# Kernel optimization log

Hardware: AMD Instinct MI355X
Metric: run time of the kernel (lower is better)

The kernel has to match this reference:

```python
import jax, jax.numpy as jnp
import numpy as np

BN_EPS = 1e-3  # Keras BatchNormalization default epsilon

def _conv2d_same(x, w, b):
    # x: NHWC, w: HWIO (kh,kw,2,1)
    y = jax.lax.conv_general_dilated(x, w, window_strides=(1, 1), padding='SAME',
                                     dimension_numbers=('NHWC', 'HWIO', 'NHWC'))
    return y + b

def _zpool(t):
    # concat([max, avg], axis=-1) over channel axis -> last dim = 2
    return jnp.concatenate([jnp.max(t, axis=-1, keepdims=True),
                            jnp.mean(t, axis=-1, keepdims=True)], axis=-1)

def _att_map(t2, w, b, g, beta, mean, var):
    y = _conv2d_same(t2, w, b)
    y = (y - mean) * jax.lax.rsqrt(var + BN_EPS) * g + beta  # inference BN
    return jax.nn.sigmoid(y)

def setup_inputs() -> dict:
    key = jax.random.key(0)
    ks = jax.random.split(key, 8)
    B, H, W, C, K, RR = 32, 56, 56, 256, 7, 8
    d = {}
    d['x'] = jax.random.normal(ks[0], (B, H, W, C), dtype=jnp.float32)
    for i, kk in zip((1, 2, 3), ks[1:4]):
        d[f'conv{i}_w'] = jax.random.normal(kk, (K, K, 2, 1), dtype=jnp.float32) * 0.1
        d[f'conv{i}_b'] = jnp.zeros((1,), dtype=jnp.float32)
        d[f'bn{i}_g'] = jnp.ones((1,), dtype=jnp.float32)
        d[f'bn{i}_b'] = jnp.zeros((1,), dtype=jnp.float32)
        d[f'bn{i}_m'] = jnp.zeros((1,), dtype=jnp.float32)
        d[f'bn{i}_v'] = jnp.ones((1,), dtype=jnp.float32)
    Ch = C // RR
    d['se_w1'] = jax.random.normal(ks[4], (C, Ch), dtype=jnp.float32) * (2.0 / C) ** 0.5
    d['se_b1'] = jnp.zeros((Ch,), dtype=jnp.float32)
    d['se_w2'] = jax.random.normal(ks[5], (Ch, C), dtype=jnp.float32) * 0.05
    d['se_b2'] = jnp.zeros((C,), dtype=jnp.float32)
    return d

def reference(x, conv1_w, conv1_b, bn1_g, bn1_b, bn1_m, bn1_v,
              conv2_w, conv2_b, bn2_g, bn2_b, bn2_m, bn2_v,
              conv3_w, conv3_b, bn3_g, bn3_b, bn3_m, bn3_v,
              se_w1, se_b1, se_w2, se_b2):
    # Branch 1 (H-axis): permute (B,H,W,C)->(B,H,C,W), pool over W
    th1 = jnp.transpose(x, (0, 1, 3, 2))
    a1 = _att_map(_zpool(th1), conv1_w, conv1_b, bn1_g, bn1_b, bn1_m, bn1_v)
    br1 = jnp.transpose(th1 * a1, (0, 1, 3, 2))
    # Branch 2 (W-axis): permute (B,H,W,C)->(B,C,W,H), pool over H
    th2 = jnp.transpose(x, (0, 3, 2, 1))
    a2 = _att_map(_zpool(th2), conv2_w, conv2_b, bn2_g, bn2_b, bn2_m, bn2_v)
    br2 = jnp.transpose(th2 * a2, (0, 3, 2, 1))
    # Branch 3 (identity): pool over C
    a3 = _att_map(_zpool(x), conv3_w, conv3_b, bn3_g, bn3_b, bn3_m, bn3_v)
    br3 = x * a3
    # TriSE1: Add branches, then SE channel gating
    s = br1 + br2 + br3
    gap = jnp.mean(s, axis=(1, 2), keepdims=True)            # (B,1,1,C)
    h = jax.nn.relu(jnp.einsum('bijc,cd->bijd', gap, se_w1) + se_b1)
    cw = jax.nn.sigmoid(jnp.einsum('bijd,dc->bijc', h, se_w2) + se_b2)
    return s * cw
```

## Files before the change

### kernel.cpp

```cpp
#include <hip/hip_runtime.h>
#include <math.h>

namespace {
constexpr int B = 32, H = 56, W = 56, C = 256;
constexpr int HW  = H * W;
constexpr int WC  = W * C;
constexpr int HC  = H * C;
constexpr int HWC = H * W * C;
constexpr int CH  = 32;
constexpr float BN_EPS = 1e-3f;

__device__ __forceinline__ float sigmoidf_(float v) { return 1.0f / (1.0f + expf(-v)); }
}

__global__ __launch_bounds__(256)
void pool_all_kernel(const float* __restrict__ x,
                     float* __restrict__ pmax1, float* __restrict__ pavg1,
                     float* __restrict__ pmax2, float* __restrict__ pavg2,
                     float* __restrict__ pmax3, float* __restrict__ pavg3) {
    const int t = threadIdx.x;
    const int lane = t & 63, sub = t >> 6;
    const int c4 = lane * 4;
    __shared__ float smx[4][256];
    __shared__ float ssm[4][256];

    if (blockIdx.x < B * H) {
        const int b = blockIdx.x / H, h = blockIdx.x % H;
        const float* xp = x + (size_t)b * HWC + (size_t)h * WC + c4;
        float4 v[14];
        #pragma unroll
        for (int wq = 0; wq < 14; ++wq)
            v[wq] = *(const float4*)(xp + (wq * 4 + sub) * C);
        float4 mx = v[0], sm = v[0];
        #pragma unroll
        for (int wq = 1; wq < 14; ++wq) {
            mx.x = fmaxf(mx.x, v[wq].x); mx.y = fmaxf(mx.y, v[wq].y);
            mx.z = fmaxf(mx.z, v[wq].z); mx.w = fmaxf(mx.w, v[wq].w);
            sm.x += v[wq].x; sm.y += v[wq].y; sm.z += v[wq].z; sm.w += v[wq].w;
        }
        #pragma unroll
        for (int wq = 0; wq < 14; ++wq) {
            float m3 = fmaxf(fmaxf(v[wq].x, v[wq].y), fmaxf(v[wq].z, v[wq].w));
            float s3 = v[wq].x + v[wq].y + v[wq].z + v[wq].w;
            #pragma unroll
            for (int off = 32; off > 0; off >>= 1) {
                m3 = fmaxf(m3, __shfl_down(m3, off));
                s3 += __shfl_down(s3, off);
            }
            if (lane == 0) {
                const int w = wq * 4 + sub;
                pmax3[b * HW + h * W + w] = m3;
                pavg3[b * HW + h * W + w] = s3 * (1.0f / C);
            }
        }
        *(float4*)&smx[sub][c4] = mx;
        *(float4*)&ssm[sub][c4] = sm;
        __syncthreads();
        const float m = fmaxf(fmaxf(smx[0][t], smx[1][t]), fmaxf(smx[2][t], smx[3][t]));
        const float s = ssm[0][t] + ssm[1][t] + ssm[2][t] + ssm[3][t];
        pmax1[b * HC + h * C + t] = m;
        pavg1[b * HC + h * C + t] = s * (1.0f / W);
    } else {
        const int tt = blockIdx.x - B * H;
        const int b = tt / W, w = tt % W;
        const float* xp = x + (size_t)b * HWC + (size_t)w * C + c4;
        float4 v[14];
        #pragma unroll
        for (int i = 0; i < 14; ++i)
            v[i] = *(const float4*)(xp + (size_t)(i * 4 + sub) * WC);
        float4 mx = v[0], sm = v[0];
        #pragma unroll
        for (int i = 1; i < 14; ++i) {
            mx.x = fmaxf(mx.x, v[i].x); mx.y = fmaxf(mx.y, v[i].y);
            mx.z = fmaxf(mx.z, v[i].z); mx.w = fmaxf(mx.w, v[i].w);
            sm.x += v[i].x; sm.y += v[i].y; sm.z += v[i].z; sm.w += v[i].w;
        }
        *(float4*)&smx[sub][c4] = mx;
        *(float4*)&ssm[sub][c4] = sm;
        __syncthreads();
        const float m = fmaxf(fmaxf(smx[0][t], smx[1][t]), fmaxf(smx[2][t], smx[3][t]));
        const float s = ssm[0][t] + ssm[1][t] + ssm[2][t] + ssm[3][t];
        pmax2[(size_t)b * WC + w * C + t] = m;
        pavg2[(size_t)b * WC + w * C + t] = s * (1.0f / H);
    }
}

__global__ __launch_bounds__(256)
void conv_all_kernel(const float* __restrict__ x,
                     const float* __restrict__ pmax1, const float* __restrict__ pavg1,
                     const float* __restrict__ pmax2, const float* __restrict__ pavg2,
                     const float* __restrict__ pmax3, const float* __restrict__ pavg3,
                     const float* __restrict__ c1w, const float* __restrict__ c1b,
                     const float* __restrict__ g1,  const float* __restrict__ be1,
                     const float* __restrict__ m1,  const float* __restrict__ v1,
                     const float* __restrict__ c2w, const float* __restrict__ c2b,
                     const float* __restrict__ g2,  const float* __restrict__ be2,
                     const float* __restrict__ m2,  const float* __restrict__ v2,
                     const float* __restrict__ c3w, const float* __restrict__ c3b,
                     const float* __restrict__ g3,  const float* __restrict__ be3,
                     const float* __restrict__ m3,  const float* __restrict__ v3,
                     float* __restrict__ a1, float* __restrict__ a2t, float* __restrict__ a3,
                     float* __restrict__ gpart) {
    const int t = threadIdx.x;
    __shared__ float wg[98];
    __shared__ float2 sp[7][264];
    __shared__ float sa3[4][56];

    if (blockIdx.x < B * 14) {
        if (t < 98) wg[t] = c3w[t];
        float2 (*sp3)[66] = (float2(*)[66])sp;
        const int tt = blockIdx.x;
        const int b = tt / 14, h0 = (tt % 14) * 4;
        const float* bm = pmax3 + (size_t)b * HW;
        const float* ba = pavg3 + (size_t)b * HW;
        for (int idx = t; idx < 10 * 62; idx += 256) {
            const int r = idx / 62, col = idx % 62;
            const int hh = h0 + r - 3, ww = col - 3;
            const bool val = (hh >= 0 && hh < H && ww >= 0 && ww < W);
            const int hs = min(max(hh, 0), H - 1), wsx = min(max(ww, 0), W - 1);
            const float pm = bm[hs * W + wsx];
            const float pa = ba[hs * W + wsx];
            sp3[r][col] = val ? make_float2(pm, pa) : make_float2(0.f, 0.f);
        }
        __syncthreads();
        if (t < 224) {
            const int r = t / 56, w = t % 56;
            const float A  = rsqrtf(v3[0] + BN_EPS) * g3[0];
            const float Bc = (c3b[0] - m3[0]) * A + be3[0];
            float acc = 0.f;
            #pragma unroll
            for (int ky = 0; ky < 7; ++ky)
                #pragma unroll
                for (int kx = 0; kx < 7; ++kx) {
                    const float2 p = sp3[r + ky][w + kx];
                    acc += p.x * wg[ky * 14 + kx * 2] + p.y * wg[ky * 14 + kx * 2 + 1];
                }
            const float av = sigmoidf_(acc * A + Bc);
            a3[b * HW + (h0 + r) * W + w] = av;
            sa3[r][w] = av;
        }
        __syncthreads();
        const int lane = t & 63, sub = t >> 6;
        const int c4 = lane * 4;
        const float* xp = x + (size_t)b * HWC + (size_t)(h0 + sub) * WC + c4;
        float4 acc4 = make_float4(0.f, 0.f, 0.f, 0.f);
        #pragma unroll 8
        for (int w = 0; w < W; ++w) {
            const float4 xv = *(const float4*)(xp + w * C);
            const float a3v = sa3[sub][w];
            acc4.x += xv.x * a3v;
            acc4.y += xv.y * a3v;
            acc4.z += xv.z * a3v;
            acc4.w += xv.w * a3v;
        }
        *(float4*)(gpart + (size_t)(b * H + h0 + sub) * C + c4) = acc4;
    } else if (blockIdx.x < B * 14 + B * H) {
        if (t < 98) wg[t] = c1w[t];
        const int tt = blockIdx.x - B * 14;
        const int b = tt / H, h = tt % H;
        const float* bm = pmax1 + (size_t)b * HC;
        const float* ba = pavg1 + (size_t)b * HC;
        #pragma unroll
        for (int ky = 0; ky < 7; ++ky) {
            const int hy = h + ky - 3;
            const bool val = (hy >= 0 && hy < H);
            const int hyc = min(max(hy, 0), H - 1);
            const float lm = bm[hyc * C + t];
            const float la = ba[hyc * C + t];
            sp[ky][t + 3] = val ? make_float2(lm, la) : make_float2(0.f, 0.f);
            if (t < 3) { sp[ky][t] = make_float2(0.f, 0.f); sp[ky][261 - t] = make_float2(0.f, 0.f); }
        }
        __syncthreads();
        const float A  = rsqrtf(v1[0] + BN_EPS) * g1[0];
        const float Bc = (c1b[0] - m1[0]) * A + be1[0];
        float acc = 0.f;
        #pragma unroll
        for (int ky = 0; ky < 7; ++ky)
            #pragma unroll
            for (int kx = 0; kx < 7; ++kx) {
                const float2 p = sp[ky][t + kx];
                acc += p.x * wg[ky * 14 + kx * 2] + p.y * wg[ky * 14 + kx * 2 + 1];
            }
        a1[b * HC + h * C + t] = sigmoidf_(acc * A + Bc);
    } else {
        if (t < 98) wg[t] = c2w[t];
        const int tt = blockIdx.x - (B * 14 + B * H);
        const int b = tt / W, w = tt % W;
        #pragma unroll
        for (int kx = 0; kx < 7; ++kx) {
            const int wx = w + kx - 3;
            const bool val = (wx >= 0 && wx < W);
            const int wxc = min(max(wx, 0), W - 1);
            const float lm = pmax2[(size_t)b * WC + wxc * C + t];
            const float la = pavg2[(size_t)b * WC + wxc * C + t];
            sp[kx][t + 3] = val ? make_float2(lm, la) : make_float2(0.f, 0.f);
            if (t < 3) { sp[kx][t] = make_float2(0.f, 0.f); sp[kx][261 - t] = make_float2(0.f, 0.f); }
        }
        __syncthreads();
        const float A  = rsqrtf(v2[0] + BN_EPS) * g2[0];
        const float Bc = (c2b[0] - m2[0]) * A + be2[0];
        float acc = 0.f;
        #pragma unroll
        for (int kx = 0; kx < 7; ++kx)
            #pragma unroll
            for (int ky = 0; ky < 7; ++ky) {
                const float2 p = sp[kx][t + ky];
                acc += p.x * wg[ky * 14 + kx * 2] + p.y * wg[ky * 14 + kx * 2 + 1];
            }
        a2t[(size_t)b * WC + w * C + t] = sigmoidf_(acc * A + Bc);
    }
}

__global__ __launch_bounds__(256)
void se_kernel(const float* __restrict__ gpart,
               const float* __restrict__ a1,  const float* __restrict__ pavg1,
               const float* __restrict__ a2t, const float* __restrict__ pavg2,
               const float* __restrict__ w1, const float* __restrict__ b1,
               const float* __restrict__ w2, const float* __restrict__ b2,
               float* __restrict__ cw) {
    const int b = blockIdx.x;
    const int t = threadIdx.x;
    __shared__ float gs[C];
    __shared__ float part[8][33];
    __shared__ float hs[CH];
    const float* pa = a1    + (size_t)b * HC + t;
    const float* pv = pavg1 + (size_t)b * HC + t;
    const float* qa = a2t   + (size_t)b * WC + t;
    const float* qv = pavg2 + (size_t)b * WC + t;
    const float* gp = gpart + (size_t)b * H * C + t;
    float s1 = 0.f, s2 = 0.f, s3 = 0.f;
    #pragma unroll 8
    for (int r = 0; r < H; ++r) {
        s1 += pa[r * C] * pv[r * C];
        s2 += qa[r * C] * qv[r * C];
        s3 += gp[r * C];
    }
    gs[t] = (s1 + s2) * (1.0f / 56.0f) + s3 * (1.0f / (float)HW);
    __syncthreads();
    {
        const int d = t & 31, j = t >> 5;
        float a = 0.f;
        #pragma unroll
        for (int i = 0; i < 32; ++i) {
            const int c = j * 32 + i;
            a += gs[c] * w1[c * CH + d];
        }
        part[j][d] = a;
    }
    __syncthreads();
    if (t < CH) {
        float a = b1[t];
        #pragma unroll
        for (int j = 0; j < 8; ++j) a += part[j][t];
        hs[t] = fmaxf(a, 0.f);
    }
    __syncthreads();
    float a = b2[t];
    #pragma unroll
    for (int d = 0; d < CH; ++d) a += hs[d] * w2[d * C + t];
    cw[b * C + t] = sigmoidf_(a);
}

__global__ __launch_bounds__(256)
void out_row_kernel(const float* __restrict__ x, const float* __restrict__ a1,
                    const float* __restrict__ a2t, const float* __restrict__ a3,
                    const float* __restrict__ cw, float* __restrict__ out) {
    const int b = blockIdx.x / H, h = blockIdx.x % H;
    const int t = threadIdx.x;
    const int lane = t & 63, sub = t >> 6;
    const int c4 = lane * 4;
    const float* xp  = x   + (size_t)b * HWC + (size_t)h * WC + c4;
    const float* a2b = a2t + (size_t)b * WC + c4;
    float*       op  = out + (size_t)b * HWC + (size_t)h * WC + c4;
    const float4 a1v = *(const float4*)(a1 + b * HC + h * C + c4);
    const float4 cwv = *(const float4*)(cw + b * C + c4);
    const float* ap = a3 + b * HW + h * W + sub;
    #pragma unroll
    for (int wq = 0; wq < 14; ++wq) {
        const int off = (wq * 4 + sub) * C;
        const float4 xv  = *(const float4*)(xp  + off);
        const float4 a2v = *(const float4*)(a2b + off);
        const float a3v  = ap[wq * 4];
        float4 o;
        o.x = xv.x * (a1v.x + a2v.x + a3v) * cwv.x;
        o.y = xv.y * (a1v.y + a2v.y + a3v) * cwv.y;
        o.z = xv.z * (a1v.z + a2v.z + a3v) * cwv.z;
        o.w = xv.w * (a1v.w + a2v.w + a3v) * cwv.w;
        *(float4*)(op + off) = o;
    }
}

extern "C" void kernel_launch(void* const* d_in, const int* in_sizes, int n_in,
                              void* d_out, int out_size, void* d_ws, size_t ws_size,
                              hipStream_t stream) {
    const float* x   = (const float*)d_in[0];
    const float* c1w = (const float*)d_in[1];  const float* c1b = (const float*)d_in[2];
    const float* g1  = (const float*)d_in[3];  const float* be1 = (const float*)d_in[4];
    const float* m1  = (const float*)d_in[5];  const float* v1  = (const float*)d_in[6];
    const float* c2w = (const float*)d_in[7];  const float* c2b = (const float*)d_in[8];
    const float* g2  = (const float*)d_in[9];  const float* be2 = (const float*)d_in[10];
    const float* m2  = (const float*)d_in[11]; const float* v2  = (const float*)d_in[12];
    const float* c3w = (const float*)d_in[13]; const float* c3b = (const float*)d_in[14];
    const float* g3  = (const float*)d_in[15]; const float* be3 = (const float*)d_in[16];
    const float* m3  = (const float*)d_in[17]; const float* v3  = (const float*)d_in[18];
    const float* sw1 = (const float*)d_in[19]; const float* sb1 = (const float*)d_in[20];
    const float* sw2 = (const float*)d_in[21]; const float* sb2 = (const float*)d_in[22];

    float* ws = (float*)d_ws;
    float* pmax1 = ws;
    float* pavg1 = pmax1 + (size_t)B * HC;
    float* pmax2 = pavg1 + (size_t)B * HC;
    float* pavg2 = pmax2 + (size_t)B * WC;
    float* pmax3 = pavg2 + (size_t)B * WC;
    float* pavg3 = pmax3 + (size_t)B * HW;
    float* a1    = pavg3 + (size_t)B * HW;
    float* a2t   = a1    + (size_t)B * HC;
    float* a3    = a2t   + (size_t)B * WC;
    float* gpart = a3    + (size_t)B * HW;
    float* cwv   = gpart + (size_t)B * H * C;

    pool_all_kernel<<<B * H + B * W, 256, 0, stream>>>(x, pmax1, pavg1, pmax2, pavg2, pmax3, pavg3);
    conv_all_kernel<<<B * 14 + B * H + B * W, 256, 0, stream>>>(
        x, pmax1, pavg1, pmax2, pavg2, pmax3, pavg3,
        c1w, c1b, g1, be1, m1, v1,
        c2w, c2b, g2, be2, m2, v2,
        c3w, c3b, g3, be3, m3, v3,
        a1, a2t, a3, gpart);
    se_kernel<<<B, 256, 0, stream>>>(gpart, a1, pavg1, a2t, pavg2, sw1, sb1, sw2, sb2, cwv);
    out_row_kernel<<<B * H, 256, 0, stream>>>(x, a1, a2t, a3, cwv, (float*)d_out);
}
```

Measured before the change: 287.4 us.

## Fuse four kernels into one cooperative persistent kernel with grid syncs

Replaces the four separate launches (pool, conv, SE, output) with a single cooperative kernel of 768 persistent blocks. Each stage loops over virtual block indices and the stages are separated by grid-wide syncs. The point is to remove per-launch overhead and the gaps between kernels. The costs are grid-barrier latency, fewer resident blocks per stage, and the SE stage running on only 32 blocks while the rest wait. If the cooperative launch fails, it falls back to the original four launches.

New measurement: 592.3 us. 2.06x slower.

```diff
diff --git a/kernel.cpp b/kernel.cpp
--- a/kernel.cpp
+++ b/kernel.cpp
@@ -1,5 +1,8 @@
 #include <hip/hip_runtime.h>
+#include <hip/hip_cooperative_groups.h>
 #include <math.h>
+
+namespace cg = cooperative_groups;
 
 namespace {
 constexpr int B = 32, H = 56, W = 56, C = 256;
@@ -9,24 +12,30 @@
 constexpr int HWC = H * W * C;
 constexpr int CH  = 32;
 constexpr float BN_EPS = 1e-3f;
+constexpr int GRID = 768;
 
 __device__ __forceinline__ float sigmoidf_(float v) { return 1.0f / (1.0f + expf(-v)); }
-}
-
-__global__ __launch_bounds__(256)
-void pool_all_kernel(const float* __restrict__ x,
-                     float* __restrict__ pmax1, float* __restrict__ pavg1,
-                     float* __restrict__ pmax2, float* __restrict__ pavg2,
-                     float* __restrict__ pmax3, float* __restrict__ pavg3) {
+
+struct Params {
+    const float *x;
+    const float *c1w, *c1b, *g1, *be1, *m1, *v1;
+    const float *c2w, *c2b, *g2, *be2, *m2, *v2;
+    const float *c3w, *c3b, *g3, *be3, *m3, *v3;
+    const float *sw1, *sb1, *sw2, *sb2;
+    float *pmax1, *pavg1, *pmax2, *pavg2, *pmax3, *pavg3;
+    float *a1, *a2t, *a3, *gpart, *cw, *out;
+};
+
+__device__ __forceinline__ void pool_body(int vb, const Params& p) {
     const int t = threadIdx.x;
     const int lane = t & 63, sub = t >> 6;
     const int c4 = lane * 4;
     __shared__ float smx[4][256];
     __shared__ float ssm[4][256];
 
-    if (blockIdx.x < B * H) {
-        const int b = blockIdx.x / H, h = blockIdx.x % H;
-        const float* xp = x + (size_t)b * HWC + (size_t)h * WC + c4;
+    if (vb < B * H) {
+        const int b = vb / H, h = vb % H;
+        const float* xp = p.x + (size_t)b * HWC + (size_t)h * WC + c4;
         float4 v[14];
         #pragma unroll
         for (int wq = 0; wq < 14; ++wq)
@@ -49,8 +58,8 @@
             }
             if (lane == 0) {
                 const int w = wq * 4 + sub;
-                pmax3[b * HW + h * W + w] = m3;
-                pavg3[b * HW + h * W + w] = s3 * (1.0f / C);
+                p.pmax3[b * HW + h * W + w] = m3;
+                p.pavg3[b * HW + h * W + w] = s3 * (1.0f / C);
             }
         }
         *(float4*)&smx[sub][c4] = mx;
@@ -58,12 +67,12 @@
         __syncthreads();
         const float m = fmaxf(fmaxf(smx[0][t], smx[1][t]), fmaxf(smx[2][t], smx[3][t]));
         const float s = ssm[0][t] + ssm[1][t] + ssm[2][t] + ssm[3][t];
-        pmax1[b * HC + h * C + t] = m;
-        pavg1[b * HC + h * C + t] = s * (1.0f / W);
+        p.pmax1[b * HC + h * C + t] = m;
+        p.pavg1[b * HC + h * C + t] = s * (1.0f / W);
     } else {
-        const int tt = blockIdx.x - B * H;
+        const int tt = vb - B * H;
         const int b = tt / W, w = tt % W;
-        const float* xp = x + (size_t)b * HWC + (size_t)w * C + c4;
+        const float* xp = p.x + (size_t)b * HWC + (size_t)w * C + c4;
         float4 v[14];
         #pragma unroll
         for (int i = 0; i < 14; ++i)
@@ -80,39 +89,23 @@
         __syncthreads();
         const float m = fmaxf(fmaxf(smx[0][t], smx[1][t]), fmaxf(smx[2][t], smx[3][t]));
         const float s = ssm[0][t] + ssm[1][t] + ssm[2][t] + ssm[3][t];
-        pmax2[(size_t)b * WC + w * C + t] = m;
-        pavg2[(size_t)b * WC + w * C + t] = s * (1.0f / H);
-    }
-}
-
-__global__ __launch_bounds__(256)
-void conv_all_kernel(const float* __restrict__ x,
-                     const float* __restrict__ pmax1, const float* __restrict__ pavg1,
-                     const float* __restrict__ pmax2, const float* __restrict__ pavg2,
-                     const float* __restrict__ pmax3, const float* __restrict__ pavg3,
-                     const float* __restrict__ c1w, const float* __restrict__ c1b,
-                     const float* __restrict__ g1,  const float* __restrict__ be1,
-                     const float* __restrict__ m1,  const float* __restrict__ v1,
-                     const float* __restrict__ c2w, const float* __restrict__ c2b,
-                     const float* __restrict__ g2,  const float* __restrict__ be2,
-                     const float* __restrict__ m2,  const float* __restrict__ v2,
-                     const float* __restrict__ c3w, const float* __restrict__ c3b,
-                     const float* __restrict__ g3,  const float* __restrict__ be3,
-                     const float* __restrict__ m3,  const float* __restrict__ v3,
-                     float* __restrict__ a1, float* __restrict__ a2t, float* __restrict__ a3,
-                     float* __restrict__ gpart) {
+        p.pmax2[(size_t)b * WC + w * C + t] = m;
+        p.pavg2[(size_t)b * WC + w * C + t] = s * (1.0f / H);
+    }
+}
+
+__device__ __forceinline__ void conv_body(int vb, const Params& p) {
     const int t = threadIdx.x;
     __shared__ float wg[98];
     __shared__ float2 sp[7][264];
     __shared__ float sa3[4][56];
 
-    if (blockIdx.x < B * 14) {
-        if (t < 98) wg[t] = c3w[t];
+    if (vb < B * 14) {
+        if (t < 98) wg[t] = p.c3w[t];
         float2 (*sp3)[66] = (float2(*)[66])sp;
-        const int tt = blockIdx.x;
-        const int b = tt / 14, h0 = (tt % 14) * 4;
-        const float* bm = pmax3 + (size_t)b * HW;
-        const float* ba = pavg3 + (size_t)b * HW;
+        const int b = vb / 14, h0 = (vb % 14) * 4;
+        const float* bm = p.pmax3 + (size_t)b * HW;
+        const float* ba = p.pavg3 + (size_t)b * HW;
         for (int idx = t; idx < 10 * 62; idx += 256) {
             const int r = idx / 62, col = idx % 62;
             const int hh = h0 + r - 3, ww = col - 3;
@@ -125,24 +118,24 @@
         __syncthreads();
         if (t < 224) {
             const int r = t / 56, w = t % 56;
-            const float A  = rsqrtf(v3[0] + BN_EPS) * g3[0];
-            const float Bc = (c3b[0] - m3[0]) * A + be3[0];
+            const float A  = rsqrtf(p.v3[0] + BN_EPS) * p.g3[0];
+            const float Bc = (p.c3b[0] - p.m3[0]) * A + p.be3[0];
             float acc = 0.f;
             #pragma unroll
             for (int ky = 0; ky < 7; ++ky)
                 #pragma unroll
                 for (int kx = 0; kx < 7; ++kx) {
-                    const float2 p = sp3[r + ky][w + kx];
-                    acc += p.x * wg[ky * 14 + kx * 2] + p.y * wg[ky * 14 + kx * 2 + 1];
+                    const float2 pv = sp3[r + ky][w + kx];
+                    acc += pv.x * wg[ky * 14 + kx * 2] + pv.y * wg[ky * 14 + kx * 2 + 1];
                 }
             const float av = sigmoidf_(acc * A + Bc);
-            a3[b * HW + (h0 + r) * W + w] = av;
+            p.a3[b * HW + (h0 + r) * W + w] = av;
             sa3[r][w] = av;
         }
         __syncthreads();
         const int lane = t & 63, sub = t >> 6;
         const int c4 = lane * 4;
-        const float* xp = x + (size_t)b * HWC + (size_t)(h0 + sub) * WC + c4;
+        const float* xp = p.x + (size_t)b * HWC + (size_t)(h0 + sub) * WC + c4;
         float4 acc4 = make_float4(0.f, 0.f, 0.f, 0.f);
         #pragma unroll 8
         for (int w = 0; w < W; ++w) {
@@ -153,13 +146,13 @@
             acc4.z += xv.z * a3v;
             acc4.w += xv.w * a3v;
         }
-        *(float4*)(gpart + (size_t)(b * H + h0 + sub) * C + c4) = acc4;
-    } else if (blockIdx.x < B * 14 + B * H) {
-        if (t < 98) wg[t] = c1w[t];
-        const int tt = blockIdx.x - B * 14;
+        *(float4*)(p.gpart + (size_t)(b * H + h0 + sub) * C + c4) = acc4;
+    } else if (vb < B * 14 + B * H) {
+        if (t < 98) wg[t] = p.c1w[t];
+        const int tt = vb - B * 14;
         const int b = tt / H, h = tt % H;
-        const float* bm = pmax1 + (size_t)b * HC;
-        const float* ba = pavg1 + (size_t)b * HC;
+        const float* bm = p.pmax1 + (size_t)b * HC;
+        const float* ba = p.pavg1 + (size_t)b * HC;
         #pragma unroll
         for (int ky = 0; ky < 7; ++ky) {
             const int hy = h + ky - 3;
@@ -171,63 +164,56 @@
             if (t < 3) { sp[ky][t] = make_float2(0.f, 0.f); sp[ky][261 - t] = make_float2(0.f, 0.f); }
         }
         __syncthreads();
-        const float A  = rsqrtf(v1[0] + BN_EPS) * g1[0];
-        const float Bc = (c1b[0] - m1[0]) * A + be1[0];
+        const float A  = rsqrtf(p.v1[0] + BN_EPS) * p.g1[0];
+        const float Bc = (p.c1b[0] - p.m1[0]) * A + p.be1[0];
         float acc = 0.f;
         #pragma unroll
         for (int ky = 0; ky < 7; ++ky)
             #pragma unroll
             for (int kx = 0; kx < 7; ++kx) {
-                const float2 p = sp[ky][t + kx];
-                acc += p.x * wg[ky * 14 + kx * 2] + p.y * wg[ky * 14 + kx * 2 + 1];
+                const float2 pv = sp[ky][t + kx];
+                acc += pv.x * wg[ky * 14 + kx * 2] + pv.y * wg[ky * 14 + kx * 2 + 1];
             }
-        a1[b * HC + h * C + t] = sigmoidf_(acc * A + Bc);
+        p.a1[b * HC + h * C + t] = sigmoidf_(acc * A + Bc);
     } else {
-        if (t < 98) wg[t] = c2w[t];
-        const int tt = blockIdx.x - (B * 14 + B * H);
+        if (t < 98) wg[t] = p.c2w[t];
+        const int tt = vb - (B * 14 + B * H);
         const int b = tt / W, w = tt % W;
         #pragma unroll
         for (int kx = 0; kx < 7; ++kx) {
             const int wx = w + kx - 3;
             const bool val = (wx >= 0 && wx < W);
             const int wxc = min(max(wx, 0), W - 1);
-            const float lm = pmax2[(size_t)b * WC + wxc * C + t];
-            const float la = pavg2[(size_t)b * WC + wxc * C + t];
+            const float lm = p.pmax2[(size_t)b * WC + wxc * C + t];
+            const float la = p.pavg2[(size_t)b * WC + wxc * C + t];
             sp[kx][t + 3] = val ? make_float2(lm, la) : make_float2(0.f, 0.f);
             if (t < 3) { sp[kx][t] = make_float2(0.f, 0.f); sp[kx][261 - t] = make_float2(0.f, 0.f); }
         }
         __syncthreads();
-        const float A  = rsqrtf(v2[0] + BN_EPS) * g2[0];
-        const float Bc = (c2b[0] - m2[0]) * A + be2[0];
+        const float A  = rsqrtf(p.v2[0] + BN_EPS) * p.g2[0];
+        const float Bc = (p.c2b[0] - p.m2[0]) * A + p.be2[0];
         float acc = 0.f;
         #pragma unroll
         for (int kx = 0; kx < 7; ++kx)
             #pragma unroll
             for (int ky = 0; ky < 7; ++ky) {
-                const float2 p = sp[kx][t + ky];
-                acc += p.x * wg[ky * 14 + kx * 2] + p.y * wg[ky * 14 + kx * 2 + 1];
+                const float2 pv = sp[kx][t + ky];
+                acc += pv.x * wg[ky * 14 + kx * 2] + pv.y * wg[ky * 14 + kx * 2 + 1];
             }
-        a2t[(size_t)b * WC + w * C + t] = sigmoidf_(acc * A + Bc);
-    }
-}
-
-__global__ __launch_bounds__(256)
-void se_kernel(const float* __restrict__ gpart,
-               const float* __restrict__ a1,  const float* __restrict__ pavg1,
-               const float* __restrict__ a2t, const float* __restrict__ pavg2,
-               const float* __restrict__ w1, const float* __restrict__ b1,
-               const float* __restrict__ w2, const float* __restrict__ b2,
-               float* __restrict__ cw) {
-    const int b = blockIdx.x;
+        p.a2t[(size_t)b * WC + w * C + t] = sigmoidf_(acc * A + Bc);
+    }
+}
+
+__device__ __forceinline__ void se_body(int b, const Params& p) {
     const int t = threadIdx.x;
     __shared__ float gs[C];
-    __shared__ float part[8][33];
+    __shared__ float prt[8][33];
     __shared__ float hs[CH];
-    const float* pa = a1    + (size_t)b * HC + t;
-    const float* pv = pavg1 + (size_t)b * HC + t;
-    const float* qa = a2t   + (size_t)b * WC + t;
-    const float* qv = pavg2 + (size_t)b * WC + t;
-    const float* gp = gpart + (size_t)b * H * C + t;
+    const float* pa = p.a1    + (size_t)b * HC + t;
+    const float* pv = p.pavg1 + (size_t)b * HC + t;
+    const float* qa = p.a2t   + (size_t)b * WC + t;
+    const float* qv = p.pavg2 + (size_t)b * WC + t;
+    const float* gp = p.gpart + (size_t)b * H * C + t;
     float s1 = 0.f, s2 = 0.f, s3 = 0.f;
     #pragma unroll 8
     for (int r = 0; r < H; ++r) {
@@ -243,38 +229,35 @@
         #pragma unroll
         for (int i = 0; i < 32; ++i) {
             const int c = j * 32 + i;
-            a += gs[c] * w1[c * CH + d];
-        }
-        part[j][d] = a;
+            a += gs[c] * p.sw1[c * CH + d];
+        }
+        prt[j][d] = a;
     }
     __syncthreads();
     if (t < CH) {
-        float a = b1[t];
-        #pragma unroll
-        for (int j = 0; j < 8; ++j) a += part[j][t];
+        float a = p.sb1[t];
+        #pragma unroll
+        for (int j = 0; j < 8; ++j) a += prt[j][t];
         hs[t] = fmaxf(a, 0.f);
     }
     __syncthreads();
-    float a = b2[t];
+    float a = p.sb2[t];
     #pragma unroll
-    for (int d = 0; d < CH; ++d) a += hs[d] * w2[d * C + t];
-    cw[b * C + t] = sigmoidf_(a);
-}
-
-__global__ __launch_bounds__(256)
-void out_row_kernel(const float* __restrict__ x, const float* __restrict__ a1,
-                    const float* __restrict__ a2t, const float* __restrict__ a3,
-                    const float* __restrict__ cw, float* __restrict__ out) {
-    const int b = blockIdx.x / H, h = blockIdx.x % H;
+    for (int d = 0; d < CH; ++d) a += hs[d] * p.sw2[d * C + t];
+    p.cw[b * C + t] = sigmoidf_(a);
+}
+
+__device__ __forceinline__ void out_body(int vb, const Params& p) {
+    const int b = vb / H, h = vb % H;
     const int t = threadIdx.x;
     const int lane = t & 63, sub = t >> 6;
     const int c4 = lane * 4;
-    const float* xp  = x   + (size_t)b * HWC + (size_t)h * WC + c4;
-    const float* a2b = a2t + (size_t)b * WC + c4;
-    float*       op  = out + (size_t)b * HWC + (size_t)h * WC + c4;
-    const float4 a1v = *(const float4*)(a1 + b * HC + h * C + c4);
-    const float4 cwv = *(const float4*)(cw + b * C + c4);
-    const float* ap = a3 + b * HW + h * W + sub;
+    const float* xp  = p.x   + (size_t)b * HWC + (size_t)h * WC + c4;
+    const float* a2b = p.a2t + (size_t)b * WC + c4;
+    float*       op  = p.out + (size_t)b * HWC + (size_t)h * WC + c4;
+    const float4 a1v = *(const float4*)(p.a1 + b * HC + h * C + c4);
+    const float4 cwv = *(const float4*)(p.cw + b * C + c4);
+    const float* ap = p.a3 + b * HW + h * W + sub;
     #pragma unroll
     for (int wq = 0; wq < 14; ++wq) {
         const int off = (wq * 4 + sub) * C;
@@ -290,42 +273,77 @@
     }
 }
 
+__global__ __launch_bounds__(256, 4)
+void mega_kernel(Params p) {
+    cg::grid_group g = cg::this_grid();
+    for (int vb = blockIdx.x; vb < B * H + B * W; vb += GRID) {
+        __syncthreads();
+        pool_body(vb, p);
+    }
+    g.sync();
+    for (int vb = blockIdx.x; vb < B * 14 + B * H + B * W; vb += GRID) {
+        __syncthreads();
+        conv_body(vb, p);
+    }
+    g.sync();
+    if (blockIdx.x < B) se_body(blockIdx.x, p);
+    g.sync();
+    for (int vb = blockIdx.x; vb < B * H; vb += GRID)
+        out_body(vb, p);
+}
+
+__global__ __launch_bounds__(256)
+void pool_all_kernel(Params p) { pool_body(blockIdx.x, p); }
+
+__global__ __launch_bounds__(256)
+void conv_all_kernel(Params p) { conv_body(blockIdx.x, p); }
+
+__global__ __launch_bounds__(256)
+void se_kernel(Params p) { se_body(blockIdx.x, p); }
+
+__global__ __launch_bounds__(256)
+void out_row_kernel(Params p) { out_body(blockIdx.x, p); }
+
+}
+
 extern "C" void kernel_launch(void* const* d_in, const int* in_sizes, int n_in,
                               void* d_out, int out_size, void* d_ws, size_t ws_size,
                               hipStream_t stream) {
-    const float* x   = (const float*)d_in[0];
-    const float* c1w = (const float*)d_in[1];  const float* c1b = (const float*)d_in[2];
-    const float* g1  = (const float*)d_in[3];  const float* be1 = (const float*)d_in[4];
-    const float* m1  = (const float*)d_in[5];  const float* v1  = (const float*)d_in[6];
-    const float* c2w = (const float*)d_in[7];  const float* c2b = (const float*)d_in[8];
-    const float* g2  = (const float*)d_in[9];  const float* be2 = (const float*)d_in[10];
-    const float* m2  = (const float*)d_in[11]; const float* v2  = (const float*)d_in[12];
-    const float* c3w = (const float*)d_in[13]; const float* c3b = (const float*)d_in[14];
-    const float* g3  = (const float*)d_in[15]; const float* be3 = (const float*)d_in[16];
-    const float* m3  = (const float*)d_in[17]; const float* v3  = (const float*)d_in[18];
-    const float* sw1 = (const float*)d_in[19]; const float* sb1 = (const float*)d_in[20];
-    const float* sw2 = (const float*)d_in[21]; const float* sb2 = (const float*)d_in[22];
+    Params hp;
+    hp.x   = (const float*)d_in[0];
+    hp.c1w = (const float*)d_in[1];  hp.c1b = (const float*)d_in[2];
+    hp.g1  = (const float*)d_in[3];  hp.be1 = (const float*)d_in[4];
+    hp.m1  = (const float*)d_in[5];  hp.v1  = (const float*)d_in[6];
+    hp.c2w = (const float*)d_in[7];  hp.c2b = (const float*)d_in[8];
+    hp.g2  = (const float*)d_in[9];  hp.be2 = (const float*)d_in[10];
+    hp.m2  = (const float*)d_in[11]; hp.v2  = (const float*)d_in[12];
+    hp.c3w = (const float*)d_in[13]; hp.c3b = (const float*)d_in[14];
+    hp.g3  = (const float*)d_in[15]; hp.be3 = (const float*)d_in[16];
+    hp.m3  = (const float*)d_in[17]; hp.v3  = (const float*)d_in[18];
+    hp.sw1 = (const float*)d_in[19]; hp.sb1 = (const float*)d_in[20];
+    hp.sw2 = (const float*)d_in[21]; hp.sb2 = (const float*)d_in[22];
 
     float* ws = (float*)d_ws;
-    float* pmax1 = ws;
-    float* pavg1 = pmax1 + (size_t)B * HC;
-    float* pmax2 = pavg1 + (size_t)B * HC;
-    float* pavg2 = pmax2 + (size_t)B * WC;
-    float* pmax3 = pavg2 + (size_t)B * WC;
-    float* pavg3 = pmax3 + (size_t)B * HW;
-    float* a1    = pavg3 + (size_t)B * HW;
-    float* a2t   = a1    + (size_t)B * HC;
-    float* a3    = a2t   + (size_t)B * WC;
-    float* gpart = a3    + (size_t)B * HW;
-    float* cwv   = gpart + (size_t)B * H * C;
-
-    pool_all_kernel<<<B * H + B * W, 256, 0, stream>>>(x, pmax1, pavg1, pmax2, pavg2, pmax3, pavg3);
-    conv_all_kernel<<<B * 14 + B * H + B * W, 256, 0, stream>>>(
-        x, pmax1, pavg1, pmax2, pavg2, pmax3, pavg3,
-        c1w, c1b, g1, be1, m1, v1,
-        c2w, c2b, g2, be2, m2, v2,
-        c3w, c3b, g3, be3, m3, v3,
-        a1, a2t, a3, gpart);
-    se_kernel<<<B, 256, 0, stream>>>(gpart, a1, pavg1, a2t, pavg2, sw1, sb1, sw2, sb2, cwv);
-    out_row_kernel<<<B * H, 256, 0, stream>>>(x, a1, a2t, a3, cwv, (float*)d_out);
-}
+    hp.pmax1 = ws;
+    hp.pavg1 = hp.pmax1 + (size_t)B * HC;
+    hp.pmax2 = hp.pavg1 + (size_t)B * HC;
+    hp.pavg2 = hp.pmax2 + (size_t)B * WC;
+    hp.pmax3 = hp.pavg2 + (size_t)B * WC;
+    hp.pavg3 = hp.pmax3 + (size_t)B * HW;
+    hp.a1    = hp.pavg3 + (size_t)B * HW;
+    hp.a2t   = hp.a1    + (size_t)B * HC;
+    hp.a3    = hp.a2t   + (size_t)B * WC;
+    hp.gpart = hp.a3    + (size_t)B * HW;
+    hp.cw    = hp.gpart + (size_t)B * H * C;
+    hp.out   = (float*)d_out;
+
+    void* kargs[] = { (void*)&hp };
+    hipError_t err = hipLaunchCooperativeKernel(mega_kernel, dim3(GRID), dim3(256),
+                                                kargs, 0, stream);
+    if (err != hipSuccess) {
+        pool_all_kernel<<<B * H + B * W, 256, 0, stream>>>(hp);
+        conv_all_kernel<<<B * 14 + B * H + B * W, 256, 0, stream>>>(hp);
+        se_kernel<<<B, 256, 0, stream>>>(hp);
+        out_row_kernel<<<B * H, 256, 0, stream>>>(hp);
+    }
+}
```
